# Kernel optimization log

Measured on AMD Instinct MI355X. Metric: run time of the kernel, lower is better.

Reference implementation:

```python
import jax, jax.numpy as jnp
import numpy as np

B, L, K = 4096, 2048, 100
CLASSNUM = 2048
OFFSET = 1172  # ((L+K-1)*2-1 + K-1 - CLASSNUM) // 2 = (4392-2048)//2


def setup_inputs() -> dict:
    key = jax.random.key(0)
    ks = jax.random.split(key, 6)
    return {
        "x_real": jax.random.normal(ks[0], (B, L), jnp.float32),
        "x_imag": jax.random.normal(ks[1], (B, L), jnp.float32),
        "w1_real": jax.random.normal(ks[2], (K,), jnp.float32) * 0.1,
        "w1_imag": jax.random.normal(ks[3], (K,), jnp.float32) * 0.1,
        "wl_real": jax.random.normal(ks[4], (K,), jnp.float32) * 0.1,
        "wl_imag": jax.random.normal(ks[5], (K,), jnp.float32) * 0.1,
    }


def _conv_full_corr(x, w):
    # torch F.conv1d(x, w, padding=K-1): full cross-correlation.
    # jnp.convolve flips its 2nd arg (true convolution), so pre-flip w.
    return jax.vmap(lambda r: jnp.convolve(r, w[::-1], mode="full"))(x)


def _self_convolution(x):
    # convolution_std: F.conv1d(x, flip(x), padding=L-1) == true self-convolution
    # out[n] = sum_j x[j] * x[n-j]  (complex multiply, no conjugate)
    return jax.vmap(lambda r: jnp.convolve(r, r, mode="full"))(x)


def reference(x_real, x_imag, w1_real, w1_imag, wl_real, wl_imag):
    x = jax.lax.complex(x_real, x_imag)    # (B, 2048) complex64
    w1 = jax.lax.complex(w1_real, w1_imag)
    wl = jax.lax.complex(wl_real, wl_imag)
    x1 = _conv_full_corr(x, w1)            # (B, 2147)
    x1 = _self_convolution(x1)             # (B, 4293)
    x2 = _conv_full_corr(x1, wl)           # (B, 4392)
    return jnp.abs(x2[:, OFFSET:OFFSET + CLASSNUM])  # (B, 2048) float32
```

## Files before the change

### kernel.cpp

```cpp
#include <hip/hip_runtime.h>
#include <math.h>

#define NFFT  4096
#define LROW  2048
#define GLEN  298
#define HLEN  199
#define OFF   1172
#define NEG2PI_D (-6.283185307179586476925286766559)
#define NEG2PI_F (-6.28318530717958647692f)
#define RSQ2  0.70710678118654752440f

__device__ __forceinline__ int pad2(int i) { return i + (i >> 4); }

__device__ __forceinline__ float2 cadd(float2 a, float2 b) { return make_float2(a.x + b.x, a.y + b.y); }
__device__ __forceinline__ float2 csub(float2 a, float2 b) { return make_float2(a.x - b.x, a.y - b.y); }
__device__ __forceinline__ float2 cmul(float2 a, float2 b) {
  return make_float2(a.x * b.x - a.y * b.y, a.x * b.y + a.y * b.x);
}
__device__ __forceinline__ float2 cmni(float2 a) { return make_float2(a.y, -a.x); }

__device__ __forceinline__ void dft4(float2 a, float2 b, float2 c, float2 d,
                                     float2& F0, float2& F1, float2& F2, float2& F3) {
  const float2 s0 = cadd(a, c), s1 = csub(a, c);
  const float2 s2 = cadd(b, d), s3 = cmni(csub(b, d));
  F0 = cadd(s0, s2); F1 = cadd(s1, s3); F2 = csub(s0, s2); F3 = csub(s1, s3);
}

__device__ __forceinline__ void bf8(const float2 c[8], float2 e[8]) {
  float2 E0, E1, E2, E3, O0, O1, O2, O3;
  dft4(c[0], c[2], c[4], c[6], E0, E1, E2, E3);
  dft4(c[1], c[3], c[5], c[7], O0, O1, O2, O3);
  const float2 u0 = O0;
  const float2 u1 = make_float2(RSQ2 * (O1.x + O1.y), RSQ2 * (O1.y - O1.x));
  const float2 u2 = cmni(O2);
  const float2 u3 = make_float2(RSQ2 * (O3.y - O3.x), -RSQ2 * (O3.x + O3.y));
  e[0] = cadd(E0, u0); e[4] = csub(E0, u0);
  e[1] = cadd(E1, u1); e[5] = csub(E1, u1);
  e[2] = cadd(E2, u2); e[6] = csub(E2, u2);
  e[3] = cadd(E3, u3); e[7] = csub(E3, u3);
}

__global__ __launch_bounds__(256)
void prep_g_kernel(const float* __restrict__ w1r, const float* __restrict__ w1i,
                   const float* __restrict__ wlr, const float* __restrict__ wli,
                   float2* __restrict__ G) {
  __shared__ float hr[HLEN], hs[HLEN], gr[GLEN], gi[GLEN];
  const int tid = threadIdx.x;
  for (int n = tid; n < HLEN; n += 256) {
    float sr = 0.f, si = 0.f;
    const int lo = n > 99 ? n - 99 : 0;
    const int hh = n < 99 ? n : 99;
    for (int i = lo; i <= hh; ++i) {
      const float ar = w1r[99 - i],       ai = w1i[99 - i];
      const float br = w1r[99 - (n - i)], bi = w1i[99 - (n - i)];
      sr += ar * br - ai * bi;
      si += ar * bi + ai * br;
    }
    hr[n] = sr; hs[n] = si;
  }
  __syncthreads();
  for (int n = tid; n < GLEN; n += 256) {
    float sr = 0.f, si = 0.f;
    const int lo = n > 99 ? n - 99 : 0;
    const int hh = n < 198 ? n : 198;
    for (int i = lo; i <= hh; ++i) {
      const float ar = hr[i],             ai = hs[i];
      const float br = wlr[99 - (n - i)], bi = wli[99 - (n - i)];
      sr += ar * br - ai * bi;
      si += ar * bi + ai * br;
    }
    gr[n] = sr; gi[n] = si;
  }
  __syncthreads();
  const int k = blockIdx.x * 256 + tid;
  double s, c;
  sincos(NEG2PI_D * (double)k / (double)NFFT, &s, &c);
  double cr = 1.0, ci = 0.0, accr = 0.0, acci = 0.0;
  for (int m = 0; m < GLEN; ++m) {
    const double a = (double)gr[m], b = (double)gi[m];
    accr += a * cr - b * ci;
    acci += a * ci + b * cr;
    const double t = cr * c - ci * s;
    ci = cr * s + ci * c;
    cr = t;
  }
  const double inv = 1.0 / (double)NFFT;
  G[k] = make_float2((float)(accr * inv), (float)(acci * inv));
}

template <int SH>
__device__ __forceinline__ void mid_stage(const float2* __restrict__ S,
                                          float2* __restrict__ D,
                                          const float2* __restrict__ Tw, int b) {
  float2 c[8];
  #pragma unroll
  for (int t = 0; t < 8; ++t) c[t] = S[pad2(b + (t << 9))];
  float2 e[8];
  bf8(c, e);
  const int M = 1 << SH;
  const int j = b >> SH;
  const int k = b & (M - 1);
  const float2 w  = Tw[b & ~(M - 1)];
  const float2 w2 = cmul(w, w);
  const float2 w3 = cmul(w2, w);
  const float2 w4 = cmul(w2, w2);
  const float2 w5 = cmul(w2, w3);
  const float2 w6 = cmul(w3, w3);
  const float2 w7 = cmul(w3, w4);
  const int base = k + (j << (SH + 3));
  D[pad2(base)]           = e[0];
  D[pad2(base + M)]       = cmul(w,  e[1]);
  D[pad2(base + 2 * M)]   = cmul(w2, e[2]);
  D[pad2(base + 3 * M)]   = cmul(w3, e[3]);
  D[pad2(base + 4 * M)]   = cmul(w4, e[4]);
  D[pad2(base + 5 * M)]   = cmul(w5, e[5]);
  D[pad2(base + 6 * M)]   = cmul(w6, e[6]);
  D[pad2(base + 7 * M)]   = cmul(w7, e[7]);
}

__global__ __launch_bounds__(512, 4)
void fft_conv_kernel(const float* __restrict__ xr, const float* __restrict__ xi,
                     const float2* __restrict__ G, float* __restrict__ out) {
  __shared__ float2 A[4352], Bb[4352];
  __shared__ float2 Tw[512];
  const int b = threadIdx.x;
  const int row = blockIdx.x;

  {
    float s, c;
    sincosf(NEG2PI_F * (float)b * (1.0f / (float)NFFT), &s, &c);
    Tw[b] = make_float2(c, s);
  }
  __syncthreads();

  {
    const float* xrr = xr + (size_t)row * LROW;
    const float* xir = xi + (size_t)row * LROW;
    float2 c[8];
    #pragma unroll
    for (int t = 0; t < 4; ++t) c[t] = make_float2(xrr[b + (t << 9)], xir[b + (t << 9)]);
    #pragma unroll
    for (int t = 4; t < 8; ++t) c[t] = make_float2(0.f, 0.f);
    float2 e[8];
    bf8(c, e);
    const float2 w  = Tw[b];
    const float2 w2 = cmul(w, w),  w3 = cmul(w2, w), w4 = cmul(w2, w2);
    const float2 w5 = cmul(w2, w3), w6 = cmul(w3, w3), w7 = cmul(w3, w4);
    const int base = b << 3;
    A[pad2(base)]     = e[0];
    A[pad2(base + 1)] = cmul(w,  e[1]);
    A[pad2(base + 2)] = cmul(w2, e[2]);
    A[pad2(base + 3)] = cmul(w3, e[3]);
    A[pad2(base + 4)] = cmul(w4, e[4]);
    A[pad2(base + 5)] = cmul(w5, e[5]);
    A[pad2(base + 6)] = cmul(w6, e[6]);
    A[pad2(base + 7)] = cmul(w7, e[7]);
  }
  __syncthreads();
  mid_stage<3>(A, Bb, Tw, b);  __syncthreads();
  mid_stage<6>(Bb, A, Tw, b);  __syncthreads();

  {
    float2 c[8];
    #pragma unroll
    for (int t = 0; t < 8; ++t) c[t] = A[pad2(b + (t << 9))];
    float2 e[8];
    bf8(c, e);
    #pragma unroll
    for (int t = 0; t < 8; ++t) {
      const int idx = b + (t << 9);
      const float2 x = e[t];
      const float2 x2 = make_float2(x.x * x.x - x.y * x.y, 2.f * x.x * x.y);
      const float2 z = cmul(x2, G[idx]);
      Bb[pad2(idx)] = make_float2(z.x, -z.y);
    }
  }
  __syncthreads();
  mid_stage<0>(Bb, A, Tw, b);  __syncthreads();
  mid_stage<3>(A, Bb, Tw, b);  __syncthreads();
  mid_stage<6>(Bb, A, Tw, b);  __syncthreads();

  {
    float2 c[8];
    #pragma unroll
    for (int t = 0; t < 8; ++t) c[t] = A[pad2(b + (t << 9))];
    float2 e[8];
    bf8(c, e);
    float* orow = out + (size_t)row * LROW;
    if (b >= 148) orow[b + 1024 - OFF] = sqrtf(e[2].x * e[2].x + e[2].y * e[2].y);
    orow[b + 1536 - OFF] = sqrtf(e[3].x * e[3].x + e[3].y * e[3].y);
    orow[b + 2048 - OFF] = sqrtf(e[4].x * e[4].x + e[4].y * e[4].y);
    orow[b + 2560 - OFF] = sqrtf(e[5].x * e[5].x + e[5].y * e[5].y);
    if (b < 148)  orow[b + 3072 - OFF] = sqrtf(e[6].x * e[6].x + e[6].y * e[6].y);
  }
}

extern "C" void kernel_launch(void* const* d_in, const int* in_sizes, int n_in,
                              void* d_out, int out_size, void* d_ws, size_t ws_size,
                              hipStream_t stream) {
  const float* xr  = (const float*)d_in[0];
  const float* xi  = (const float*)d_in[1];
  const float* w1r = (const float*)d_in[2];
  const float* w1i = (const float*)d_in[3];
  const float* wlr = (const float*)d_in[4];
  const float* wli = (const float*)d_in[5];
  float* out = (float*)d_out;
  float2* G = (float2*)d_ws;
  const int rows = in_sizes[0] / LROW;

  prep_g_kernel<<<NFFT / 256, 256, 0, stream>>>(w1r, w1i, wlr, wli, G);
  fft_conv_kernel<<<rows, 512, 0, stream>>>(xr, xi, G, out);
}
```

Before: 180.1 us.

## Switch FFT to in-place single-buffer DIF/DIT with permuted spectrum filter

Reworks the FFT convolution so the forward transform is decimation-in-frequency and the inverse is decimation-in-time, both done in place in one shared buffer. The ping-pong buffer goes away and LDS per block is halved. The filter spectrum is stored in digit-reversed order so the pointwise multiply reads contiguous float4 values, and the last forward stage, the multiply and the first inverse stage are fused in registers. Launch bounds are raised to allow twice as many blocks per CU, which risks register pressure or spills.

```diff
diff --git a/kernel.cpp b/kernel.cpp
--- a/kernel.cpp
+++ b/kernel.cpp
@@ -43,7 +43,7 @@
 __global__ __launch_bounds__(256)
 void prep_g_kernel(const float* __restrict__ w1r, const float* __restrict__ w1i,
                    const float* __restrict__ wlr, const float* __restrict__ wli,
-                   float2* __restrict__ G) {
+                   float2* __restrict__ Ghat) {
   __shared__ float hr[HLEN], hs[HLEN], gr[GLEN], gi[GLEN];
   const int tid = threadIdx.x;
   for (int n = tid; n < HLEN; n += 256) {
@@ -85,43 +85,42 @@
     cr = t;
   }
   const double inv = 1.0 / (double)NFFT;
-  G[k] = make_float2((float)(accr * inv), (float)(acci * inv));
-}
-
-template <int SH>
-__device__ __forceinline__ void mid_stage(const float2* __restrict__ S,
-                                          float2* __restrict__ D,
-                                          const float2* __restrict__ Tw, int b) {
+  const int p = ((k & 7) << 9) | (((k >> 3) & 7) << 6) | (((k >> 6) & 7) << 3) | (k >> 9);
+  Ghat[p] = make_float2((float)(accr * inv), (float)(acci * inv));
+}
+
+template <int SH, bool PRE>
+__device__ __forceinline__ void stage_ip(float2* A, const float2* __restrict__ Tw, int b) {
+  const int M = 1 << SH;
+  const int k = b & (M - 1);
+  const int Q = b >> SH;
+  const int base = (Q << (SH + 3)) + k;
   float2 c[8];
   #pragma unroll
-  for (int t = 0; t < 8; ++t) c[t] = S[pad2(b + (t << 9))];
+  for (int t = 0; t < 8; ++t) c[t] = A[pad2(base + (t << SH))];
+  const float2 w  = Tw[(NFFT >> (SH + 3)) * k];
+  const float2 w2 = cmul(w, w),  w3 = cmul(w2, w),  w4 = cmul(w2, w2);
+  const float2 w5 = cmul(w2, w3), w6 = cmul(w3, w3), w7 = cmul(w3, w4);
   float2 e[8];
-  bf8(c, e);
-  const int M = 1 << SH;
-  const int j = b >> SH;
-  const int k = b & (M - 1);
-  const float2 w  = Tw[b & ~(M - 1)];
-  const float2 w2 = cmul(w, w);
-  const float2 w3 = cmul(w2, w);
-  const float2 w4 = cmul(w2, w2);
-  const float2 w5 = cmul(w2, w3);
-  const float2 w6 = cmul(w3, w3);
-  const float2 w7 = cmul(w3, w4);
-  const int base = k + (j << (SH + 3));
-  D[pad2(base)]           = e[0];
-  D[pad2(base + M)]       = cmul(w,  e[1]);
-  D[pad2(base + 2 * M)]   = cmul(w2, e[2]);
-  D[pad2(base + 3 * M)]   = cmul(w3, e[3]);
-  D[pad2(base + 4 * M)]   = cmul(w4, e[4]);
-  D[pad2(base + 5 * M)]   = cmul(w5, e[5]);
-  D[pad2(base + 6 * M)]   = cmul(w6, e[6]);
-  D[pad2(base + 7 * M)]   = cmul(w7, e[7]);
-}
-
-__global__ __launch_bounds__(512, 4)
+  if (PRE) {
+    c[1] = cmul(w,  c[1]); c[2] = cmul(w2, c[2]); c[3] = cmul(w3, c[3]);
+    c[4] = cmul(w4, c[4]); c[5] = cmul(w5, c[5]); c[6] = cmul(w6, c[6]);
+    c[7] = cmul(w7, c[7]);
+    bf8(c, e);
+  } else {
+    bf8(c, e);
+    e[1] = cmul(w,  e[1]); e[2] = cmul(w2, e[2]); e[3] = cmul(w3, e[3]);
+    e[4] = cmul(w4, e[4]); e[5] = cmul(w5, e[5]); e[6] = cmul(w6, e[6]);
+    e[7] = cmul(w7, e[7]);
+  }
+  #pragma unroll
+  for (int t = 0; t < 8; ++t) A[pad2(base + (t << SH))] = e[t];
+}
+
+__global__ __launch_bounds__(512, 8)
 void fft_conv_kernel(const float* __restrict__ xr, const float* __restrict__ xi,
-                     const float2* __restrict__ G, float* __restrict__ out) {
-  __shared__ float2 A[4352], Bb[4352];
+                     const float2* __restrict__ Ghat, float* __restrict__ out) {
+  __shared__ float2 A[4351];
   __shared__ float2 Tw[512];
   const int b = threadIdx.x;
   const int row = blockIdx.x;
@@ -144,46 +143,59 @@
     float2 e[8];
     bf8(c, e);
     const float2 w  = Tw[b];
-    const float2 w2 = cmul(w, w),  w3 = cmul(w2, w), w4 = cmul(w2, w2);
+    const float2 w2 = cmul(w, w),  w3 = cmul(w2, w),  w4 = cmul(w2, w2);
     const float2 w5 = cmul(w2, w3), w6 = cmul(w3, w3), w7 = cmul(w3, w4);
+    A[pad2(b)]              = e[0];
+    A[pad2(b + (1 << 9))]   = cmul(w,  e[1]);
+    A[pad2(b + (2 << 9))]   = cmul(w2, e[2]);
+    A[pad2(b + (3 << 9))]   = cmul(w3, e[3]);
+    A[pad2(b + (4 << 9))]   = cmul(w4, e[4]);
+    A[pad2(b + (5 << 9))]   = cmul(w5, e[5]);
+    A[pad2(b + (6 << 9))]   = cmul(w6, e[6]);
+    A[pad2(b + (7 << 9))]   = cmul(w7, e[7]);
+  }
+  __syncthreads();
+  stage_ip<6, false>(A, Tw, b);  __syncthreads();
+  stage_ip<3, false>(A, Tw, b);  __syncthreads();
+
+  {
     const int base = b << 3;
-    A[pad2(base)]     = e[0];
-    A[pad2(base + 1)] = cmul(w,  e[1]);
-    A[pad2(base + 2)] = cmul(w2, e[2]);
-    A[pad2(base + 3)] = cmul(w3, e[3]);
-    A[pad2(base + 4)] = cmul(w4, e[4]);
-    A[pad2(base + 5)] = cmul(w5, e[5]);
-    A[pad2(base + 6)] = cmul(w6, e[6]);
-    A[pad2(base + 7)] = cmul(w7, e[7]);
-  }
-  __syncthreads();
-  mid_stage<3>(A, Bb, Tw, b);  __syncthreads();
-  mid_stage<6>(Bb, A, Tw, b);  __syncthreads();
-
-  {
     float2 c[8];
     #pragma unroll
-    for (int t = 0; t < 8; ++t) c[t] = A[pad2(b + (t << 9))];
+    for (int t = 0; t < 8; ++t) c[t] = A[pad2(base + t)];
     float2 e[8];
     bf8(c, e);
+    const float4* G4 = reinterpret_cast<const float4*>(Ghat + base);
+    float4 gq[4];
+    #pragma unroll
+    for (int q = 0; q < 4; ++q) gq[q] = G4[q];
     #pragma unroll
     for (int t = 0; t < 8; ++t) {
-      const int idx = b + (t << 9);
       const float2 x = e[t];
       const float2 x2 = make_float2(x.x * x.x - x.y * x.y, 2.f * x.x * x.y);
-      const float2 z = cmul(x2, G[idx]);
-      Bb[pad2(idx)] = make_float2(z.x, -z.y);
+      const float2 g = (t & 1) ? make_float2(gq[t >> 1].z, gq[t >> 1].w)
+                               : make_float2(gq[t >> 1].x, gq[t >> 1].y);
+      const float2 z = cmul(x2, g);
+      c[t] = make_float2(z.x, -z.y);
     }
-  }
-  __syncthreads();
-  mid_stage<0>(Bb, A, Tw, b);  __syncthreads();
-  mid_stage<3>(A, Bb, Tw, b);  __syncthreads();
-  mid_stage<6>(Bb, A, Tw, b);  __syncthreads();
+    bf8(c, e);
+    #pragma unroll
+    for (int t = 0; t < 8; ++t) A[pad2(base + t)] = e[t];
+  }
+  __syncthreads();
+  stage_ip<3, true>(A, Tw, b);   __syncthreads();
+  stage_ip<6, true>(A, Tw, b);   __syncthreads();
 
   {
     float2 c[8];
     #pragma unroll
     for (int t = 0; t < 8; ++t) c[t] = A[pad2(b + (t << 9))];
+    const float2 w  = Tw[b];
+    const float2 w2 = cmul(w, w),  w3 = cmul(w2, w),  w4 = cmul(w2, w2);
+    const float2 w5 = cmul(w2, w3), w6 = cmul(w3, w3), w7 = cmul(w3, w4);
+    c[1] = cmul(w,  c[1]); c[2] = cmul(w2, c[2]); c[3] = cmul(w3, c[3]);
+    c[4] = cmul(w4, c[4]); c[5] = cmul(w5, c[5]); c[6] = cmul(w6, c[6]);
+    c[7] = cmul(w7, c[7]);
     float2 e[8];
     bf8(c, e);
     float* orow = out + (size_t)row * LROW;
@@ -205,9 +217,9 @@
   const float* wlr = (const float*)d_in[4];
   const float* wli = (const float*)d_in[5];
   float* out = (float*)d_out;
-  float2* G = (float2*)d_ws;
+  float2* Ghat = (float2*)d_ws;
   const int rows = in_sizes[0] / LROW;
 
-  prep_g_kernel<<<NFFT / 256, 256, 0, stream>>>(w1r, w1i, wlr, wli, G);
-  fft_conv_kernel<<<rows, 512, 0, stream>>>(xr, xi, G, out);
-}
+  prep_g_kernel<<<NFFT / 256, 256, 0, stream>>>(w1r, w1i, wlr, wli, Ghat);
+  fft_conv_kernel<<<rows, 512, 0, stream>>>(xr, xi, Ghat, out);
+}
```

Result: slower. 207.0 us (+14.9%).
